# Kernel optimization log

Measured on AMD Instinct MI355X. Metric: run time of the kernel, lower is better.

The kernel has to match this reference:

```python
import jax, jax.numpy as jnp
import numpy as np

B, S, F_IN, F_OUT, K = 4, 4096, 64, 64, 32


def setup_inputs() -> dict:
    key = jax.random.key(0)
    k1, k2, k3 = jax.random.split(key, 3)
    X = jax.random.normal(k1, (B, S, F_IN), dtype=jnp.float32)
    M = jax.random.normal(k2, (B, S, K), dtype=jnp.float32)
    # xavier_uniform for weight: bound = sqrt(6/(fan_in+fan_out))
    bound = float(np.sqrt(6.0 / (F_IN + F_OUT)))
    weight = jax.random.uniform(k3, (F_IN, F_OUT), dtype=jnp.float32,
                                minval=-bound, maxval=bound)
    bias = jnp.zeros((F_OUT,), dtype=jnp.float32)
    return {"X": X, "M": M, "weight": weight, "bias": bias}


def reference(X, M, weight, bias):
    # similarity = softmax(relu(M M^T), axis=-1)  -> [B, S, S]
    sim_raw = jnp.einsum('bsk,btk->bst', M, M)
    sim = jax.nn.softmax(jax.nn.relu(sim_raw), axis=-1)
    # X W  -> [B, S, F_OUT]
    Xw = jnp.einsum('bsf,fo->bso', X, weight)
    # mode='add': (I + A) Xw = Xw + A @ Xw  (identity matmul folded)
    Z = Xw + jnp.einsum('bst,bto->bso', sim, Xw)
    Z = Z + bias
    # dropout is identity at inference (eval mode)
    return Z
```

## Files before the change

### kernel.cpp

```cpp
#include <hip/hip_runtime.h>
#include <cstdint>

#define BATCH  4
#define SLEN   4096
#define FDIM   64
#define KDIM   32
#define KSPLIT 8
#define CHUNK  (SLEN / KSPLIT)

typedef __attribute__((ext_vector_type(8))) short bf16x8;
typedef __attribute__((ext_vector_type(4))) short bf16x4;
typedef __attribute__((ext_vector_type(4))) float f32x4;

static __device__ __forceinline__ short f2bf(float f) {
    union { float f; unsigned u; } v; v.f = f;
    unsigned r = v.u + 0x7fffu + ((v.u >> 16) & 1u);
    return (short)(r >> 16);
}
static __device__ __forceinline__ float bf2f(short s) {
    union { unsigned u; float f; } v;
    v.u = ((unsigned)(unsigned short)s) << 16;
    return v.f;
}
static __device__ __forceinline__ unsigned pack2bf(float a, float b) {
    union { float f; unsigned u; } x, y; x.f = a; y.f = b;
    unsigned ra = x.u + 0x7fffu + ((x.u >> 16) & 1u);
    unsigned rb = y.u + 0x7fffu + ((y.u >> 16) & 1u);
    return __builtin_amdgcn_perm(rb, ra, 0x07060302u);
}

__global__ __launch_bounds__(256) void prep(const float4* __restrict__ M4,
                                            ushort4* __restrict__ H4,
                                            ushort4* __restrict__ L4,
                                            const float* __restrict__ X,
                                            const float4* __restrict__ W4,
                                            float4* __restrict__ V4,
                                            short* __restrict__ Vt) {
    const int blk = blockIdx.y * gridDim.x + blockIdx.x;
#pragma unroll
    for (int r = 0; r < 2; ++r) {
        int i = (blk * 2 + r) * 256 + threadIdx.x;
        float4 m = M4[i];
        ushort4 h, l;
        h.x = (unsigned short)f2bf(m.x); l.x = (unsigned short)f2bf(m.x - bf2f((short)h.x));
        h.y = (unsigned short)f2bf(m.y); l.y = (unsigned short)f2bf(m.y - bf2f((short)h.y));
        h.z = (unsigned short)f2bf(m.z); l.z = (unsigned short)f2bf(m.z - bf2f((short)h.z));
        h.w = (unsigned short)f2bf(m.w); l.w = (unsigned short)f2bf(m.w - bf2f((short)h.w));
        H4[i] = h; L4[i] = l;
    }
    __shared__ float t[64][65];
    const int b  = blockIdx.y;
    const int s0 = blockIdx.x * 64;
    const int o4 = threadIdx.x & 15;
    const int rq = threadIdx.x >> 4;
#pragma unroll
    for (int half = 0; half < 4; ++half) {
        int r = half * 16 + rq;
        const float* __restrict__ xr = X + ((size_t)b * SLEN + s0 + r) * FDIM;
        float4 acc = make_float4(0.f, 0.f, 0.f, 0.f);
#pragma unroll
        for (int f = 0; f < FDIM; ++f) {
            float4 w = W4[f * 16 + o4];
            float  x = xr[f];
            acc.x = fmaf(x, w.x, acc.x);
            acc.y = fmaf(x, w.y, acc.y);
            acc.z = fmaf(x, w.z, acc.z);
            acc.w = fmaf(x, w.w, acc.w);
        }
        V4[((size_t)b * SLEN + s0 + r) * 16 + o4] = acc;
        t[r][o4 * 4 + 0] = acc.x;
        t[r][o4 * 4 + 1] = acc.y;
        t[r][o4 * 4 + 2] = acc.z;
        t[r][o4 * 4 + 3] = acc.w;
    }
    __syncthreads();
    const int c0 = threadIdx.x & 63;
    const int r0 = threadIdx.x >> 6;
#pragma unroll
    for (int i = 0; i < 16; ++i) {
        int f = r0 + i * 4;
        Vt[((size_t)b * FDIM + f) * SLEN + s0 + c0] = f2bf(t[c0][f]);
    }
}

__global__ __launch_bounds__(256, 3) void attn_mfma(const short* __restrict__ Mhi,
                                                    const short* __restrict__ Mlo,
                                                    const short* __restrict__ Vt,
                                                    float* __restrict__ accP,
                                                    float* __restrict__ lP) {
    const int bid  = blockIdx.x;
    const int slab = (bid & 7) + 8 * (bid >> 8);
    const int qblk = (bid >> 3) & 31;
    const int b    = slab >> 3;
    const int ks   = slab & 7;

    const int tid  = threadIdx.x;
    const int wave = tid >> 6;
    const int lane = tid & 63;
    const int col  = lane & 15;
    const int quad = lane >> 4;
    const int qbase = qblk * 128 + wave * 32;
    const int k0    = ks * CHUNK;

    const short* __restrict__ Mbh = Mhi + (size_t)b * SLEN * KDIM;
    const short* __restrict__ Mbl = Mlo + (size_t)b * SLEN * KDIM;
    const short* __restrict__ Vb  = Vt  + (size_t)b * FDIM * SLEN;

    __shared__ short khi[32 * 40];
    __shared__ short klo[32 * 40];
    __shared__ short vsh[64 * 40];

    bf16x8 Qh[2], Ql[2];
#pragma unroll
    for (int tq = 0; tq < 2; ++tq) {
        int qo = (qbase + tq * 16 + col) * KDIM + quad * 8;
        Qh[tq] = *(const bf16x8*)(Mbh + qo);
        Ql[tq] = *(const bf16x8*)(Mbl + qo);
    }

    f32x4 accf[2][4];
#pragma unroll
    for (int tq = 0; tq < 2; ++tq)
#pragma unroll
        for (int fg = 0; fg < 4; ++fg) accf[tq][fg] = (f32x4){0.f, 0.f, 0.f, 0.f};
    float lacc[2] = {0.f, 0.f};

    const int krow  = (tid & 127) >> 2;
    const int kpart = tid & 3;
    const int vrow  = tid >> 2;
    const short* __restrict__ Msrc = (tid < 128) ? Mbh : Mbl;
    short* __restrict__ kdst = (tid < 128) ? khi : klo;

#pragma unroll 1
    for (int kt = k0; kt < k0 + CHUNK; kt += 32) {
        bf16x8 kstg = *(const bf16x8*)(Msrc + (kt + krow) * KDIM + kpart * 8);
        bf16x8 vstg = *(const bf16x8*)(Vb + (size_t)vrow * SLEN + kt + kpart * 8);
        __syncthreads();
        *(bf16x8*)(kdst + krow * 40 + kpart * 8) = kstg;
        *(bf16x8*)(vsh + vrow * 40 + kpart * 8)  = vstg;
        __syncthreads();

        bf16x8 Kh0 = *(const bf16x8*)(khi + col * 40 + quad * 8);
        bf16x8 Kh1 = *(const bf16x8*)(khi + (16 + col) * 40 + quad * 8);
        bf16x8 Kl0 = *(const bf16x8*)(klo + col * 40 + quad * 8);
        bf16x8 Kl1 = *(const bf16x8*)(klo + (16 + col) * 40 + quad * 8);

        bf16x8 Vv[4];
#pragma unroll
        for (int fg = 0; fg < 4; ++fg) {
            const short* vp = vsh + (fg * 16 + col) * 40 + quad * 4;
            bf16x4 vlo = *(const bf16x4*)(vp);
            bf16x4 vhi = *(const bf16x4*)(vp + 16);
            Vv[fg] = __builtin_shufflevector(vlo, vhi, 0, 1, 2, 3, 4, 5, 6, 7);
        }

#pragma unroll
        for (int tq = 0; tq < 2; ++tq) {
            f32x4 z = (f32x4){0.f, 0.f, 0.f, 0.f};
            f32x4 c0 = __builtin_amdgcn_mfma_f32_16x16x32_bf16(Kh0, Ql[tq], z, 0, 0, 0);
            f32x4 c1 = __builtin_amdgcn_mfma_f32_16x16x32_bf16(Kh1, Ql[tq], z, 0, 0, 0);
            c0 = __builtin_amdgcn_mfma_f32_16x16x32_bf16(Kl0, Qh[tq], c0, 0, 0, 0);
            c1 = __builtin_amdgcn_mfma_f32_16x16x32_bf16(Kl1, Qh[tq], c1, 0, 0, 0);
            c0 = __builtin_amdgcn_mfma_f32_16x16x32_bf16(Kh0, Qh[tq], c0, 0, 0, 0);
            c1 = __builtin_amdgcn_mfma_f32_16x16x32_bf16(Kh1, Qh[tq], c1, 0, 0, 0);

            float e00 = __expf(fmaxf(c0[0], 0.f));
            float e01 = __expf(fmaxf(c0[1], 0.f));
            float e02 = __expf(fmaxf(c0[2], 0.f));
            float e03 = __expf(fmaxf(c0[3], 0.f));
            float e10 = __expf(fmaxf(c1[0], 0.f));
            float e11 = __expf(fmaxf(c1[1], 0.f));
            float e12 = __expf(fmaxf(c1[2], 0.f));
            float e13 = __expf(fmaxf(c1[3], 0.f));
            lacc[tq] += ((e00 + e01) + (e02 + e03)) + ((e10 + e11) + (e12 + e13));

            union { unsigned u[4]; bf16x8 v; } pa;
            pa.u[0] = pack2bf(e00, e01);
            pa.u[1] = pack2bf(e02, e03);
            pa.u[2] = pack2bf(e10, e11);
            pa.u[3] = pack2bf(e12, e13);

#pragma unroll
            for (int fg = 0; fg < 4; ++fg)
                accf[tq][fg] = __builtin_amdgcn_mfma_f32_16x16x32_bf16(
                    pa.v, Vv[fg], accf[tq][fg], 0, 0, 0);
        }
    }

#pragma unroll
    for (int tq = 0; tq < 2; ++tq) {
#pragma unroll
        for (int j = 0; j < 4; ++j) {
            int q = qbase + tq * 16 + quad * 4 + j;
            size_t base = ((size_t)b * SLEN + q) * KSPLIT + ks;
            float* __restrict__ op = accP + base * FDIM;
#pragma unroll
            for (int fg = 0; fg < 4; ++fg)
                op[fg * 16 + col] = accf[tq][fg][j];
        }
        float lv = lacc[tq];
        lv += __shfl_xor(lv, 16);
        lv += __shfl_xor(lv, 32);
        if (quad == 0) {
            int q = qbase + tq * 16 + col;
            lP[((size_t)b * SLEN + q) * KSPLIT + ks] = lv;
        }
    }
}

__global__ __launch_bounds__(256) void combine_kernel(const float4* __restrict__ V4,
                                                      const float4* __restrict__ accP4,
                                                      const float* __restrict__ lP,
                                                      const float4* __restrict__ bias4,
                                                      float4* __restrict__ out4) {
    int i  = blockIdx.x * 256 + threadIdx.x;
    int o4 = i & 15;
    int row = i >> 4;
    float nx = 0.f, ny = 0.f, nz = 0.f, nw = 0.f, den = 0.f;
#pragma unroll
    for (int k = 0; k < KSPLIT; ++k) {
        float4 a = accP4[((size_t)row * KSPLIT + k) * 16 + o4];
        nx += a.x; ny += a.y; nz += a.z; nw += a.w;
        den += lP[(size_t)row * KSPLIT + k];
    }
    float r = 1.f / den;
    float4 v = V4[i];
    float4 bb = bias4[o4];
    float4 o;
    o.x = v.x + nx * r + bb.x;
    o.y = v.y + ny * r + bb.y;
    o.z = v.z + nz * r + bb.z;
    o.w = v.w + nw * r + bb.w;
    out4[i] = o;
}

extern "C" void kernel_launch(void* const* d_in, const int* in_sizes, int n_in,
                              void* d_out, int out_size, void* d_ws, size_t ws_size,
                              hipStream_t stream) {
    const float* X    = (const float*)d_in[0];
    const float* M    = (const float*)d_in[1];
    const float* W    = (const float*)d_in[2];
    const float* bias = (const float*)d_in[3];
    float* out = (float*)d_out;

    const size_t vElems = (size_t)BATCH * SLEN * FDIM;
    const size_t mElems = (size_t)BATCH * SLEN * KDIM;
    const size_t rows   = (size_t)BATCH * SLEN;

    float* Vf   = (float*)d_ws;
    float* accP = Vf + vElems;
    float* lP   = accP + vElems * KSPLIT;
    short* Mhi  = (short*)(lP + rows * KSPLIT);
    short* Mlo  = Mhi + mElems;
    short* Vt   = Mlo + mElems;

    prep<<<dim3(SLEN / 64, BATCH), 256, 0, stream>>>(
        (const float4*)M, (ushort4*)Mhi, (ushort4*)Mlo,
        X, (const float4*)W, (float4*)Vf, Vt);

    attn_mfma<<<dim3((SLEN / 128) * BATCH * KSPLIT), 256, 0, stream>>>(
        Mhi, Mlo, Vt, accP, lP);

    combine_kernel<<<(int)(vElems / 1024), 256, 0, stream>>>(
        (const float4*)Vf, (const float4*)accP, lP, (const float4*)bias,
        (float4*)out);
}
```

Baseline: 120.1 us.

## Double-buffer K/V tiles, widen key step to 64, permute Vt for vector LDS reads

The attention kernel now processes 64 keys per iteration with double-buffered LDS tiles. Global loads for the next tile are issued before the MFMA work on the current one, and there is one barrier per iteration instead of two. The Vt producer writes columns in a permuted order so each lane can read its V operand with a single 128-bit LDS load instead of two 64-bit loads plus a shuffle. This costs more LDS and registers, and dropping the occupancy hint of 3 in launch_bounds may lower occupancy.

```diff
diff --git a/kernel.cpp b/kernel.cpp
--- a/kernel.cpp
+++ b/kernel.cpp
@@ -9,7 +9,6 @@
 #define CHUNK  (SLEN / KSPLIT)
 
 typedef __attribute__((ext_vector_type(8))) short bf16x8;
-typedef __attribute__((ext_vector_type(4))) short bf16x4;
 typedef __attribute__((ext_vector_type(4))) float f32x4;
 
 static __device__ __forceinline__ short f2bf(float f) {
@@ -76,18 +75,20 @@
     __syncthreads();
     const int c0 = threadIdx.x & 63;
     const int r0 = threadIdx.x >> 6;
+    const int pc = (c0 & 32) | (((c0 >> 2) & 3) << 3) | (((c0 >> 4) & 1) << 2)
+                 | (c0 & 3);
 #pragma unroll
     for (int i = 0; i < 16; ++i) {
         int f = r0 + i * 4;
-        Vt[((size_t)b * FDIM + f) * SLEN + s0 + c0] = f2bf(t[c0][f]);
-    }
-}
-
-__global__ __launch_bounds__(256, 3) void attn_mfma(const short* __restrict__ Mhi,
-                                                    const short* __restrict__ Mlo,
-                                                    const short* __restrict__ Vt,
-                                                    float* __restrict__ accP,
-                                                    float* __restrict__ lP) {
+        Vt[((size_t)b * FDIM + f) * SLEN + s0 + pc] = f2bf(t[c0][f]);
+    }
+}
+
+__global__ __launch_bounds__(256) void attn_mfma(const short* __restrict__ Mhi,
+                                                 const short* __restrict__ Mlo,
+                                                 const short* __restrict__ Vt,
+                                                 float* __restrict__ accP,
+                                                 float* __restrict__ lP) {
     const int bid  = blockIdx.x;
     const int slab = (bid & 7) + 8 * (bid >> 8);
     const int qblk = (bid >> 3) & 31;
@@ -106,9 +107,9 @@
     const short* __restrict__ Mbl = Mlo + (size_t)b * SLEN * KDIM;
     const short* __restrict__ Vb  = Vt  + (size_t)b * FDIM * SLEN;
 
-    __shared__ short khi[32 * 40];
-    __shared__ short klo[32 * 40];
-    __shared__ short vsh[64 * 40];
+    __shared__ short khi[2][64 * 40];
+    __shared__ short klo[2][64 * 40];
+    __shared__ short vsh[2][2][64 * 40];
 
     bf16x8 Qh[2], Ql[2];
 #pragma unroll
@@ -125,66 +126,92 @@
         for (int fg = 0; fg < 4; ++fg) accf[tq][fg] = (f32x4){0.f, 0.f, 0.f, 0.f};
     float lacc[2] = {0.f, 0.f};
 
-    const int krow  = (tid & 127) >> 2;
-    const int kpart = tid & 3;
-    const int vrow  = tid >> 2;
-    const short* __restrict__ Msrc = (tid < 128) ? Mbh : Mbl;
-    short* __restrict__ kdst = (tid < 128) ? khi : klo;
-
+    const int srow  = tid >> 2;
+    const int spart = tid & 3;
+
+    {
+        bf16x8 rkh = *(const bf16x8*)(Mbh + (k0 + srow) * KDIM + spart * 8);
+        bf16x8 rkl = *(const bf16x8*)(Mbl + (k0 + srow) * KDIM + spart * 8);
+        bf16x8 rv0 = *(const bf16x8*)(Vb + (size_t)srow * SLEN + k0 + spart * 8);
+        bf16x8 rv1 = *(const bf16x8*)(Vb + (size_t)srow * SLEN + k0 + 32 + spart * 8);
+        *(bf16x8*)(khi[0]    + srow * 40 + spart * 8) = rkh;
+        *(bf16x8*)(klo[0]    + srow * 40 + spart * 8) = rkl;
+        *(bf16x8*)(vsh[0][0] + srow * 40 + spart * 8) = rv0;
+        *(bf16x8*)(vsh[0][1] + srow * 40 + spart * 8) = rv1;
+    }
+    __syncthreads();
+
+    int p = 0;
 #pragma unroll 1
-    for (int kt = k0; kt < k0 + CHUNK; kt += 32) {
-        bf16x8 kstg = *(const bf16x8*)(Msrc + (kt + krow) * KDIM + kpart * 8);
-        bf16x8 vstg = *(const bf16x8*)(Vb + (size_t)vrow * SLEN + kt + kpart * 8);
-        __syncthreads();
-        *(bf16x8*)(kdst + krow * 40 + kpart * 8) = kstg;
-        *(bf16x8*)(vsh + vrow * 40 + kpart * 8)  = vstg;
-        __syncthreads();
-
-        bf16x8 Kh0 = *(const bf16x8*)(khi + col * 40 + quad * 8);
-        bf16x8 Kh1 = *(const bf16x8*)(khi + (16 + col) * 40 + quad * 8);
-        bf16x8 Kl0 = *(const bf16x8*)(klo + col * 40 + quad * 8);
-        bf16x8 Kl1 = *(const bf16x8*)(klo + (16 + col) * 40 + quad * 8);
-
-        bf16x8 Vv[4];
-#pragma unroll
-        for (int fg = 0; fg < 4; ++fg) {
-            const short* vp = vsh + (fg * 16 + col) * 40 + quad * 4;
-            bf16x4 vlo = *(const bf16x4*)(vp);
-            bf16x4 vhi = *(const bf16x4*)(vp + 16);
-            Vv[fg] = __builtin_shufflevector(vlo, vhi, 0, 1, 2, 3, 4, 5, 6, 7);
-        }
+    for (int kt = k0; kt < k0 + CHUNK; kt += 64) {
+        const int ktn  = kt + 64;
+        const bool more = ktn < k0 + CHUNK;
+        bf16x8 nkh, nkl, nv0, nv1;
+        if (more) {
+            nkh = *(const bf16x8*)(Mbh + (ktn + srow) * KDIM + spart * 8);
+            nkl = *(const bf16x8*)(Mbl + (ktn + srow) * KDIM + spart * 8);
+            nv0 = *(const bf16x8*)(Vb + (size_t)srow * SLEN + ktn + spart * 8);
+            nv1 = *(const bf16x8*)(Vb + (size_t)srow * SLEN + ktn + 32 + spart * 8);
+        }
+
+        const short* __restrict__ KH = khi[p];
+        const short* __restrict__ KL = klo[p];
+        bf16x8 Kh[4], Kl[4];
+#pragma unroll
+        for (int t = 0; t < 4; ++t) {
+            Kh[t] = *(const bf16x8*)(KH + (t * 16 + col) * 40 + quad * 8);
+            Kl[t] = *(const bf16x8*)(KL + (t * 16 + col) * 40 + quad * 8);
+        }
+        bf16x8 Vv[4][2];
+#pragma unroll
+        for (int fg = 0; fg < 4; ++fg)
+#pragma unroll
+            for (int h = 0; h < 2; ++h)
+                Vv[fg][h] = *(const bf16x8*)(vsh[p][h]
+                                             + (fg * 16 + col) * 40 + quad * 8);
 
 #pragma unroll
         for (int tq = 0; tq < 2; ++tq) {
             f32x4 z = (f32x4){0.f, 0.f, 0.f, 0.f};
-            f32x4 c0 = __builtin_amdgcn_mfma_f32_16x16x32_bf16(Kh0, Ql[tq], z, 0, 0, 0);
-            f32x4 c1 = __builtin_amdgcn_mfma_f32_16x16x32_bf16(Kh1, Ql[tq], z, 0, 0, 0);
-            c0 = __builtin_amdgcn_mfma_f32_16x16x32_bf16(Kl0, Qh[tq], c0, 0, 0, 0);
-            c1 = __builtin_amdgcn_mfma_f32_16x16x32_bf16(Kl1, Qh[tq], c1, 0, 0, 0);
-            c0 = __builtin_amdgcn_mfma_f32_16x16x32_bf16(Kh0, Qh[tq], c0, 0, 0, 0);
-            c1 = __builtin_amdgcn_mfma_f32_16x16x32_bf16(Kh1, Qh[tq], c1, 0, 0, 0);
-
-            float e00 = __expf(fmaxf(c0[0], 0.f));
-            float e01 = __expf(fmaxf(c0[1], 0.f));
-            float e02 = __expf(fmaxf(c0[2], 0.f));
-            float e03 = __expf(fmaxf(c0[3], 0.f));
-            float e10 = __expf(fmaxf(c1[0], 0.f));
-            float e11 = __expf(fmaxf(c1[1], 0.f));
-            float e12 = __expf(fmaxf(c1[2], 0.f));
-            float e13 = __expf(fmaxf(c1[3], 0.f));
-            lacc[tq] += ((e00 + e01) + (e02 + e03)) + ((e10 + e11) + (e12 + e13));
-
-            union { unsigned u[4]; bf16x8 v; } pa;
-            pa.u[0] = pack2bf(e00, e01);
-            pa.u[1] = pack2bf(e02, e03);
-            pa.u[2] = pack2bf(e10, e11);
-            pa.u[3] = pack2bf(e12, e13);
-
-#pragma unroll
-            for (int fg = 0; fg < 4; ++fg)
-                accf[tq][fg] = __builtin_amdgcn_mfma_f32_16x16x32_bf16(
-                    pa.v, Vv[fg], accf[tq][fg], 0, 0, 0);
-        }
+            f32x4 c[4];
+#pragma unroll
+            for (int t = 0; t < 4; ++t) {
+                c[t] = __builtin_amdgcn_mfma_f32_16x16x32_bf16(Kh[t], Ql[tq], z, 0, 0, 0);
+                c[t] = __builtin_amdgcn_mfma_f32_16x16x32_bf16(Kl[t], Qh[tq], c[t], 0, 0, 0);
+                c[t] = __builtin_amdgcn_mfma_f32_16x16x32_bf16(Kh[t], Qh[tq], c[t], 0, 0, 0);
+            }
+#pragma unroll
+            for (int g = 0; g < 2; ++g) {
+                float e0 = __expf(fmaxf(c[2 * g][0], 0.f));
+                float e1 = __expf(fmaxf(c[2 * g][1], 0.f));
+                float e2 = __expf(fmaxf(c[2 * g][2], 0.f));
+                float e3 = __expf(fmaxf(c[2 * g][3], 0.f));
+                float e4 = __expf(fmaxf(c[2 * g + 1][0], 0.f));
+                float e5 = __expf(fmaxf(c[2 * g + 1][1], 0.f));
+                float e6 = __expf(fmaxf(c[2 * g + 1][2], 0.f));
+                float e7 = __expf(fmaxf(c[2 * g + 1][3], 0.f));
+                lacc[tq] += ((e0 + e1) + (e2 + e3)) + ((e4 + e5) + (e6 + e7));
+
+                union { unsigned u[4]; bf16x8 v; } pa;
+                pa.u[0] = pack2bf(e0, e1);
+                pa.u[1] = pack2bf(e2, e3);
+                pa.u[2] = pack2bf(e4, e5);
+                pa.u[3] = pack2bf(e6, e7);
+#pragma unroll
+                for (int fg = 0; fg < 4; ++fg)
+                    accf[tq][fg] = __builtin_amdgcn_mfma_f32_16x16x32_bf16(
+                        pa.v, Vv[fg][g], accf[tq][fg], 0, 0, 0);
+            }
+        }
+
+        if (more) {
+            *(bf16x8*)(khi[p ^ 1]    + srow * 40 + spart * 8) = nkh;
+            *(bf16x8*)(klo[p ^ 1]    + srow * 40 + spart * 8) = nkl;
+            *(bf16x8*)(vsh[p ^ 1][0] + srow * 40 + spart * 8) = nv0;
+            *(bf16x8*)(vsh[p ^ 1][1] + srow * 40 + spart * 8) = nv1;
+        }
+        __syncthreads();
+        p ^= 1;
     }
 
 #pragma unroll
```

After: 124.2 us. 3.4% more time.

## Prescale queries by log2e, use exp2, MFMA row sums, permute V layout

Applied to the files above, without the earlier changes.

The prep kernel now writes a second hi/lo bf16 split of M pre-multiplied by log2(e), used as the query operand. The attention loop can then call the native exp2 instead of __expf. The per-row softmax denominator is accumulated by an extra MFMA against a ones vector, replacing scalar adds and cross-lane shuffles. Vt columns are stored permuted so each V fragment is one 8-element LDS load instead of two 4-element loads. Occupancy hint rises from 3 to 4 blocks per CU, at the cost of extra prep work and more workspace traffic.

```diff
diff --git a/kernel.cpp b/kernel.cpp
--- a/kernel.cpp
+++ b/kernel.cpp
@@ -9,7 +9,6 @@
 #define CHUNK  (SLEN / KSPLIT)
 
 typedef __attribute__((ext_vector_type(8))) short bf16x8;
-typedef __attribute__((ext_vector_type(4))) short bf16x4;
 typedef __attribute__((ext_vector_type(4))) float f32x4;
 
 static __device__ __forceinline__ short f2bf(float f) {
@@ -32,21 +31,29 @@
 __global__ __launch_bounds__(256) void prep(const float4* __restrict__ M4,
                                             ushort4* __restrict__ H4,
                                             ushort4* __restrict__ L4,
+                                            ushort4* __restrict__ QH4,
+                                            ushort4* __restrict__ QL4,
                                             const float* __restrict__ X,
                                             const float4* __restrict__ W4,
                                             float4* __restrict__ V4,
                                             short* __restrict__ Vt) {
     const int blk = blockIdx.y * gridDim.x + blockIdx.x;
+    const float LOG2E = 1.4426950408889634f;
 #pragma unroll
     for (int r = 0; r < 2; ++r) {
         int i = (blk * 2 + r) * 256 + threadIdx.x;
         float4 m = M4[i];
-        ushort4 h, l;
+        ushort4 h, l, sh, sl;
         h.x = (unsigned short)f2bf(m.x); l.x = (unsigned short)f2bf(m.x - bf2f((short)h.x));
         h.y = (unsigned short)f2bf(m.y); l.y = (unsigned short)f2bf(m.y - bf2f((short)h.y));
         h.z = (unsigned short)f2bf(m.z); l.z = (unsigned short)f2bf(m.z - bf2f((short)h.z));
         h.w = (unsigned short)f2bf(m.w); l.w = (unsigned short)f2bf(m.w - bf2f((short)h.w));
-        H4[i] = h; L4[i] = l;
+        float sx = m.x * LOG2E, sy = m.y * LOG2E, sz = m.z * LOG2E, sw = m.w * LOG2E;
+        sh.x = (unsigned short)f2bf(sx); sl.x = (unsigned short)f2bf(sx - bf2f((short)sh.x));
+        sh.y = (unsigned short)f2bf(sy); sl.y = (unsigned short)f2bf(sy - bf2f((short)sh.y));
+        sh.z = (unsigned short)f2bf(sz); sl.z = (unsigned short)f2bf(sz - bf2f((short)sh.z));
+        sh.w = (unsigned short)f2bf(sw); sl.w = (unsigned short)f2bf(sw - bf2f((short)sh.w));
+        H4[i] = h; L4[i] = l; QH4[i] = sh; QL4[i] = sl;
     }
     __shared__ float t[64][65];
     const int b  = blockIdx.y;
@@ -76,15 +83,19 @@
     __syncthreads();
     const int c0 = threadIdx.x & 63;
     const int r0 = threadIdx.x >> 6;
+    const int pc = (c0 & 32) | (((c0 >> 2) & 3) << 3) | (((c0 >> 4) & 1) << 2)
+                 | (c0 & 3);
 #pragma unroll
     for (int i = 0; i < 16; ++i) {
         int f = r0 + i * 4;
-        Vt[((size_t)b * FDIM + f) * SLEN + s0 + c0] = f2bf(t[c0][f]);
-    }
-}
-
-__global__ __launch_bounds__(256, 3) void attn_mfma(const short* __restrict__ Mhi,
+        Vt[((size_t)b * FDIM + f) * SLEN + s0 + pc] = f2bf(t[c0][f]);
+    }
+}
+
+__global__ __launch_bounds__(256, 4) void attn_mfma(const short* __restrict__ Mhi,
                                                     const short* __restrict__ Mlo,
+                                                    const short* __restrict__ Qhi,
+                                                    const short* __restrict__ Qlo,
                                                     const short* __restrict__ Vt,
                                                     float* __restrict__ accP,
                                                     float* __restrict__ lP) {
@@ -104,6 +115,8 @@
 
     const short* __restrict__ Mbh = Mhi + (size_t)b * SLEN * KDIM;
     const short* __restrict__ Mbl = Mlo + (size_t)b * SLEN * KDIM;
+    const short* __restrict__ Qbh = Qhi + (size_t)b * SLEN * KDIM;
+    const short* __restrict__ Qbl = Qlo + (size_t)b * SLEN * KDIM;
     const short* __restrict__ Vb  = Vt  + (size_t)b * FDIM * SLEN;
 
     __shared__ short khi[32 * 40];
@@ -114,16 +127,20 @@
 #pragma unroll
     for (int tq = 0; tq < 2; ++tq) {
         int qo = (qbase + tq * 16 + col) * KDIM + quad * 8;
-        Qh[tq] = *(const bf16x8*)(Mbh + qo);
-        Ql[tq] = *(const bf16x8*)(Mbl + qo);
-    }
-
-    f32x4 accf[2][4];
-#pragma unroll
-    for (int tq = 0; tq < 2; ++tq)
+        Qh[tq] = *(const bf16x8*)(Qbh + qo);
+        Ql[tq] = *(const bf16x8*)(Qbl + qo);
+    }
+
+    const bf16x8 ONES = (bf16x8){0x3F80, 0x3F80, 0x3F80, 0x3F80,
+                                 0x3F80, 0x3F80, 0x3F80, 0x3F80};
+
+    f32x4 accf[2][4], accl[2];
+#pragma unroll
+    for (int tq = 0; tq < 2; ++tq) {
+        accl[tq] = (f32x4){0.f, 0.f, 0.f, 0.f};
 #pragma unroll
         for (int fg = 0; fg < 4; ++fg) accf[tq][fg] = (f32x4){0.f, 0.f, 0.f, 0.f};
-    float lacc[2] = {0.f, 0.f};
+    }
 
     const int krow  = (tid & 127) >> 2;
     const int kpart = tid & 3;
@@ -144,15 +161,10 @@
         bf16x8 Kh1 = *(const bf16x8*)(khi + (16 + col) * 40 + quad * 8);
         bf16x8 Kl0 = *(const bf16x8*)(klo + col * 40 + quad * 8);
         bf16x8 Kl1 = *(const bf16x8*)(klo + (16 + col) * 40 + quad * 8);
-
         bf16x8 Vv[4];
 #pragma unroll
-        for (int fg = 0; fg < 4; ++fg) {
-            const short* vp = vsh + (fg * 16 + col) * 40 + quad * 4;
-            bf16x4 vlo = *(const bf16x4*)(vp);
-            bf16x4 vhi = *(const bf16x4*)(vp + 16);
-            Vv[fg] = __builtin_shufflevector(vlo, vhi, 0, 1, 2, 3, 4, 5, 6, 7);
-        }
+        for (int fg = 0; fg < 4; ++fg)
+            Vv[fg] = *(const bf16x8*)(vsh + (fg * 16 + col) * 40 + quad * 8);
 
 #pragma unroll
         for (int tq = 0; tq < 2; ++tq) {
@@ -164,22 +176,23 @@
             c0 = __builtin_amdgcn_mfma_f32_16x16x32_bf16(Kh0, Qh[tq], c0, 0, 0, 0);
             c1 = __builtin_amdgcn_mfma_f32_16x16x32_bf16(Kh1, Qh[tq], c1, 0, 0, 0);
 
-            float e00 = __expf(fmaxf(c0[0], 0.f));
-            float e01 = __expf(fmaxf(c0[1], 0.f));
-            float e02 = __expf(fmaxf(c0[2], 0.f));
-            float e03 = __expf(fmaxf(c0[3], 0.f));
-            float e10 = __expf(fmaxf(c1[0], 0.f));
-            float e11 = __expf(fmaxf(c1[1], 0.f));
-            float e12 = __expf(fmaxf(c1[2], 0.f));
-            float e13 = __expf(fmaxf(c1[3], 0.f));
-            lacc[tq] += ((e00 + e01) + (e02 + e03)) + ((e10 + e11) + (e12 + e13));
+            float e0 = __builtin_amdgcn_exp2f(fmaxf(c0[0], 0.f));
+            float e1 = __builtin_amdgcn_exp2f(fmaxf(c0[1], 0.f));
+            float e2 = __builtin_amdgcn_exp2f(fmaxf(c0[2], 0.f));
+            float e3 = __builtin_amdgcn_exp2f(fmaxf(c0[3], 0.f));
+            float e4 = __builtin_amdgcn_exp2f(fmaxf(c1[0], 0.f));
+            float e5 = __builtin_amdgcn_exp2f(fmaxf(c1[1], 0.f));
+            float e6 = __builtin_amdgcn_exp2f(fmaxf(c1[2], 0.f));
+            float e7 = __builtin_amdgcn_exp2f(fmaxf(c1[3], 0.f));
 
             union { unsigned u[4]; bf16x8 v; } pa;
-            pa.u[0] = pack2bf(e00, e01);
-            pa.u[1] = pack2bf(e02, e03);
-            pa.u[2] = pack2bf(e10, e11);
-            pa.u[3] = pack2bf(e12, e13);
-
+            pa.u[0] = pack2bf(e0, e1);
+            pa.u[1] = pack2bf(e2, e3);
+            pa.u[2] = pack2bf(e4, e5);
+            pa.u[3] = pack2bf(e6, e7);
+
+            accl[tq] = __builtin_amdgcn_mfma_f32_16x16x32_bf16(pa.v, ONES,
+                                                               accl[tq], 0, 0, 0);
 #pragma unroll
             for (int fg = 0; fg < 4; ++fg)
                 accf[tq][fg] = __builtin_amdgcn_mfma_f32_16x16x32_bf16(
@@ -197,13 +210,7 @@
 #pragma unroll
             for (int fg = 0; fg < 4; ++fg)
                 op[fg * 16 + col] = accf[tq][fg][j];
-        }
-        float lv = lacc[tq];
-        lv += __shfl_xor(lv, 16);
-        lv += __shfl_xor(lv, 32);
-        if (quad == 0) {
-            int q = qbase + tq * 16 + col;
-            lP[((size_t)b * SLEN + q) * KSPLIT + ks] = lv;
+            if (col == 0) lP[base] = accl[tq][j];
         }
     }
 }
@@ -252,14 +259,17 @@
     float* lP   = accP + vElems * KSPLIT;
     short* Mhi  = (short*)(lP + rows * KSPLIT);
     short* Mlo  = Mhi + mElems;
-    short* Vt   = Mlo + mElems;
+    short* Qhi  = Mlo + mElems;
+    short* Qlo  = Qhi + mElems;
+    short* Vt   = Qlo + mElems;
 
     prep<<<dim3(SLEN / 64, BATCH), 256, 0, stream>>>(
         (const float4*)M, (ushort4*)Mhi, (ushort4*)Mlo,
+        (ushort4*)Qhi, (ushort4*)Qlo,
         X, (const float4*)W, (float4*)Vf, Vt);
 
     attn_mfma<<<dim3((SLEN / 128) * BATCH * KSPLIT), 256, 0, stream>>>(
-        Mhi, Mlo, Vt, accP, lP);
+        Mhi, Mlo, Qhi, Qlo, Vt, accP, lP);
 
     combine_kernel<<<(int)(vElems / 1024), 256, 0, stream>>>(
         (const float4*)Vf, (const float4*)accP, lP, (const float4*)bias,
```

After: 122.5 us. About the same (+2.0%).
